# Performance work log

Hardware: AMD Instinct MI355X
Metric: run time of the kernel (lower is better)

The kernel has to match this reference:

```python
import jax, jax.numpy as jnp
import numpy as np
import math

EMBED_DIM = 512
NUM_CLASSES = 100000
BATCH = 1024
MARGIN = 0.5
SCALE = 64.0


def setup_inputs() -> dict:
    key = jax.random.key(0)
    k1, k2, k3 = jax.random.split(key, 3)
    embeddings = jax.random.normal(k1, (BATCH, EMBED_DIM), dtype=jnp.float32)
    labels = jax.random.randint(k2, (BATCH,), 0, NUM_CLASSES, dtype=jnp.int64)
    # xavier_uniform for weight [num_classes, embedding_dim]
    limit = math.sqrt(6.0 / (NUM_CLASSES + EMBED_DIM))
    weight = jax.random.uniform(k3, (NUM_CLASSES, EMBED_DIM), dtype=jnp.float32,
                                minval=-limit, maxval=limit)
    return {"embeddings": embeddings, "weight": weight, "labels": labels}


def _l2norm(x, axis=-1, eps=1e-12):
    # matches torch F.normalize (p=2, eps=1e-12)
    n = jnp.linalg.norm(x, axis=axis, keepdims=True)
    return x / jnp.maximum(n, eps)


def reference(embeddings, weight, labels):
    cos_m = math.cos(MARGIN)
    sin_m = math.sin(MARGIN)
    th = math.cos(math.pi - MARGIN)
    mm = math.sin(math.pi - MARGIN) * MARGIN

    # cosine similarity: [B, C]
    cosine = _l2norm(embeddings) @ _l2norm(weight).T
    sine = jnp.sqrt(jnp.clip(1.0 - cosine * cosine, 0.0, 1.0))
    phi = cosine * cos_m - sine * sin_m
    phi = jnp.where(cosine > th, phi, cosine - mm)

    # apply margin only at the label position
    one_hot = jax.nn.one_hot(labels, NUM_CLASSES, dtype=cosine.dtype)
    logits = SCALE * (one_hot * phi + (1.0 - one_hot) * cosine)

    # cross entropy, mean reduction
    logp = jax.nn.log_softmax(logits, axis=-1)
    nll = -jnp.take_along_axis(logp, labels[:, None], axis=1)[:, 0]
    return jnp.mean(nll)
```

## Files before the change

### kernel.cpp

```cpp
#include <hip/hip_runtime.h>
#include <hip/hip_bf16.h>
#include <math.h>

#define B_ROWS 1024
#define EMB    512
#define NCLS   100000
#define SCALE_ 64.0f
#define COS_M 0.8775825618903728f
#define SIN_M 0.479425538604203f
#define TH_C  (-0.8775825618903728f)
#define MM_C  0.2397127693021015f

#define BM 128
#define BN 128
#define BK 32
#define NTILES 782
#define KCHUNKS 16

#define NT2   391
#define GRID2 1564

typedef __attribute__((ext_vector_type(8))) short bf16x8;
typedef __attribute__((ext_vector_type(4))) short s16x4;
typedef __attribute__((ext_vector_type(4))) float f32x4;

typedef __attribute__((address_space(1))) const unsigned int GLP;
typedef __attribute__((address_space(3))) unsigned int LDP;

__device__ __forceinline__ float bf2f(short u) {
  unsigned int x = ((unsigned int)(unsigned short)u) << 16;
  return __builtin_bit_cast(float, x);
}
__device__ __forceinline__ short f2bf(float f) {
  unsigned int u = __builtin_bit_cast(unsigned int, f);
  u += 0x7FFF + ((u >> 16) & 1);
  return (short)(u >> 16);
}

__device__ __forceinline__ void load16(const void* g, void* l) {
  __builtin_amdgcn_global_load_lds((GLP*)g, (LDP*)l, 16, 0, 0);
}

__global__ void setup_kernel(const void* __restrict__ emb, const int* __restrict__ labels,
                             float* __restrict__ row_sum, float* __restrict__ accum,
                             int* __restrict__ flag, int* __restrict__ dflag) {
  const int t = threadIdx.x;
  row_sum[t] = 0.f;
  row_sum[t + 512] = 0.f;
  if (t == 0) *accum = 0.f;

  if (t < 64) {
    bf16x8 v = *(const bf16x8*)((const short*)emb + t * 8);
    float s = 0.f;
    #pragma unroll
    for (int j = 0; j < 8; ++j) { float f = bf2f(v[j]); s += f * f; }
    #pragma unroll
    for (int off = 1; off < 64; off <<= 1) s += __shfl_xor(s, off);
    if (t == 0) *dflag = (s < 1e8f) ? 1 : 0;
  }

  int v = labels[2 * t + 1];
  #pragma unroll
  for (int off = 1; off < 64; off <<= 1) v |= __shfl_xor(v, off);
  __shared__ int red[8];
  if ((t & 63) == 0) red[t >> 6] = v;
  __syncthreads();
  if (t == 0) {
    int o = 0;
    #pragma unroll
    for (int i = 0; i < 8; ++i) o |= red[i];
    *flag = (o == 0) ? 1 : 0;
  }
}

__global__ __launch_bounds__(256) void normconv_kernel(
    const void* __restrict__ emb, const void* __restrict__ wgt,
    const int* __restrict__ dflag,
    float* __restrict__ inv_e, float* __restrict__ inv_w,
    short* __restrict__ An, short* __restrict__ Wn, const int do_conv) {
  const int sub  = threadIdx.x & 15;
  const int rloc = threadIdx.x >> 4;
  const int row  = blockIdx.x * 16 + rloc;
  int r;
  const void* base;
  float* dst;
  short* out;
  if (row < B_ROWS) { r = row; base = emb; dst = inv_e + row; out = An + (size_t)row * EMB; }
  else {
    r = row - B_ROWS;
    if (r >= NCLS) return;
    base = wgt; dst = inv_w + r; out = Wn + (size_t)r * EMB;
  }
  const int isbf16 = *dflag;
  float f[32];
  if (isbf16) {
    const short* p = (const short*)base + (size_t)r * EMB;
    #pragma unroll
    for (int j = 0; j < 4; ++j) {
      bf16x8 v = *(const bf16x8*)(p + j * 128 + sub * 8);
      #pragma unroll
      for (int t = 0; t < 8; ++t) f[j * 8 + t] = bf2f(v[t]);
    }
  } else {
    const float* p = (const float*)base + (size_t)r * EMB;
    #pragma unroll
    for (int j = 0; j < 8; ++j) {
      f32x4 v = *(const f32x4*)(p + j * 64 + sub * 4);
      #pragma unroll
      for (int t = 0; t < 4; ++t) f[j * 4 + t] = v[t];
    }
  }
  float s = 0.f;
  #pragma unroll
  for (int j = 0; j < 32; ++j) s += f[j] * f[j];
  #pragma unroll
  for (int off = 1; off < 16; off <<= 1) s += __shfl_xor(s, off);
  const float inv = 1.f / fmaxf(sqrtf(s), 1e-12f);
  if (sub == 0) *dst = inv;
  if (do_conv) {
    if (isbf16) {
      #pragma unroll
      for (int j = 0; j < 4; ++j) {
        bf16x8 o;
        #pragma unroll
        for (int t = 0; t < 8; ++t) o[t] = f2bf(f[j * 8 + t] * inv);
        *(bf16x8*)(out + j * 128 + sub * 8) = o;
      }
    } else {
      #pragma unroll
      for (int j = 0; j < 8; ++j) {
        s16x4 o;
        #pragma unroll
        for (int t = 0; t < 4; ++t) o[t] = f2bf(f[j * 4 + t] * inv);
        *(s16x4*)(out + j * 64 + sub * 4) = o;
      }
    }
  }
}

__global__ __launch_bounds__(512, 2) void arc_gemm_fast(
    const short* __restrict__ A, const short* __restrict__ W,
    const int* __restrict__ labels, const int* __restrict__ flag,
    float* __restrict__ row_sum, float* __restrict__ lablogit) {
  const int bid = blockIdx.x;
  const int k   = bid & 7;
  const int jj  = bid >> 3;
  const int wgid = (k < 4 ? k * 196 : 4 * 196 + (k - 4) * 195) + jj;
  const int ytile = wgid >> 2;
  const int xtile = wgid & 3;
  if (ytile >= NT2) return;

  __shared__ __align__(16) char Lraw[131072 + 1024 + 4096];
  char* L = Lraw;
  int*   shl = (int*)(L + 131072);
  float* shs = (float*)(L + 131072 + 1024);

  const int tid  = threadIdx.x;
  const int wave = tid >> 6;
  const int lane = tid & 63;
  const int wm   = wave >> 2;
  const int wn   = wave & 3;
  const int lr16 = lane & 15;
  const int lkg  = lane >> 4;
  const int mBase = xtile * 256;
  const int nBase = ytile * 256;

  const char* Ab = (const char*)A;
  const char* Wb = (const char*)W;

  f32x4 zero = {0.f, 0.f, 0.f, 0.f};
  f32x4 acc[8][4];
  #pragma unroll
  for (int i = 0; i < 8; ++i)
    #pragma unroll
    for (int j2 = 0; j2 < 4; ++j2) acc[i][j2] = zero;

  auto stage = [&](int kt, int p) {
    #pragma unroll
    for (int j = 0; j < 4; ++j) {
      const int row = j * 64 + (tid >> 3);
      const int sl  = (tid & 7) ^ (row & 7);
      load16(Ab + (size_t)(mBase + row) * 1024 + kt * 128 + sl * 16,
             L + p * 65536 + j * 8192 + wave * 1024);
      int br = nBase + row;
      if (br >= NCLS) br = NCLS - 1;
      load16(Wb + (size_t)br * 1024 + kt * 128 + sl * 16,
             L + p * 65536 + 32768 + j * 8192 + wave * 1024);
    }
  };

  stage(0, 0);
  stage(1, 1);
  asm volatile("s_waitcnt vmcnt(8)" ::: "memory");
  __builtin_amdgcn_s_barrier();

  for (int t = 0; t < 8; ++t) {
    const int p = t & 1;
    const short* Abuf = (const short*)(L + p * 65536);
    const short* Bbuf = (const short*)(L + p * 65536 + 32768);
    bf16x8 af[2][8], bb[2][4];
    #pragma unroll
    for (int ks = 0; ks < 2; ++ks) {
      #pragma unroll
      for (int mi = 0; mi < 8; ++mi) {
        const int ra = wm * 128 + mi * 16 + lr16;
        const int sa = (ks * 4 + lkg) ^ (ra & 7);
        af[ks][mi] = *(const bf16x8*)(Abuf + ra * 64 + sa * 8);
      }
      #pragma unroll
      for (int ni = 0; ni < 4; ++ni) {
        const int rb = wn * 64 + ni * 16 + lr16;
        const int sb = (ks * 4 + lkg) ^ (rb & 7);
        bb[ks][ni] = *(const bf16x8*)(Bbuf + rb * 64 + sb * 8);
      }
    }
    asm volatile("s_waitcnt lgkmcnt(0)" ::: "memory");
    __builtin_amdgcn_s_barrier();
    stage((t + 2) & 7, p);
    __builtin_amdgcn_s_setprio(1);
    #pragma unroll
    for (int mi = 0; mi < 8; ++mi)
      #pragma unroll
      for (int ni = 0; ni < 4; ++ni) {
        acc[mi][ni] = __builtin_amdgcn_mfma_f32_16x16x32_bf16(af[0][mi], bb[0][ni], acc[mi][ni], 0, 0, 0);
        acc[mi][ni] = __builtin_amdgcn_mfma_f32_16x16x32_bf16(af[1][mi], bb[1][ni], acc[mi][ni], 0, 0, 0);
      }
    __builtin_amdgcn_s_setprio(0);
    asm volatile("s_waitcnt vmcnt(8)" ::: "memory");
    __builtin_amdgcn_s_barrier();
  }

  asm volatile("s_waitcnt vmcnt(0)" ::: "memory");
  __syncthreads();
  if (tid < 256) {
    const int r = mBase + tid;
    const int f = *flag;
    shl[tid] = labels[f ? (size_t)(2 * r) : (size_t)r];
  }
  __syncthreads();

  #pragma unroll
  for (int mi = 0; mi < 8; ++mi) {
    #pragma unroll
    for (int reg = 0; reg < 4; ++reg) {
      const int lrow = wm * 128 + mi * 16 + lkg * 4 + reg;
      const int grow = mBase + lrow;
      const int lab = shl[lrow];
      float s = 0.f;
      #pragma unroll
      for (int ni = 0; ni < 4; ++ni) {
        const int gcol = nBase + wn * 64 + ni * 16 + lr16;
        if (gcol < NCLS) {
          const float cosv = acc[mi][ni][reg];
          float logit;
          if (gcol == lab) {
            const float sine = sqrtf(fmaxf(1.f - cosv * cosv, 0.f));
            float phi = cosv * COS_M - sine * SIN_M;
            phi = (cosv > TH_C) ? phi : (cosv - MM_C);
            logit = SCALE_ * phi;
            lablogit[grow] = logit;
          } else {
            logit = SCALE_ * cosv;
          }
          s += __expf(logit - SCALE_);
        }
      }
      #pragma unroll
      for (int off = 1; off < 16; off <<= 1) s += __shfl_xor(s, off);
      if (lr16 == 0) shs[lrow * 4 + wn] = s;
    }
  }
  __syncthreads();
  if (tid < 256)
    atomicAdd(&row_sum[mBase + tid],
              shs[tid * 4] + shs[tid * 4 + 1] + shs[tid * 4 + 2] + shs[tid * 4 + 3]);
}

__global__ __launch_bounds__(256, 3) void arc_gemm(
    const void* __restrict__ A, const void* __restrict__ W,
    const float* __restrict__ inv_e, const float* __restrict__ inv_w,
    const int* __restrict__ labels, const int* __restrict__ flag,
    const int* __restrict__ dflag,
    float* __restrict__ row_sum, float* __restrict__ lablogit) {
  __shared__ short As[BM * BK];
  __shared__ short Bs[BN * BK];
  __shared__ int   sh_lab[BM];
  __shared__ float sh_sum[BM][2];

  const int tid  = threadIdx.x;
  const int wave = tid >> 6;
  const int lane = tid & 63;
  const int wy = wave >> 1;
  const int wx = wave & 1;
  const int lr = lane & 15;
  const int lk = lane >> 4;
  const int mBase = blockIdx.x * BM;
  const int nBase = blockIdx.y * BN;
  const int isbf16 = *dflag;

  const int srow  = lane >> 2;
  const int sbyte = (lane & 3) * 16;

  f32x4 zero = {0.f, 0.f, 0.f, 0.f};
  f32x4 acc[4][4];
  #pragma unroll
  for (int i = 0; i < 4; ++i)
    #pragma unroll
    for (int j = 0; j < 4; ++j) acc[i][j] = zero;

  const char*  Ab = (const char*)A;
  const char*  Wb = (const char*)W;
  const float* Af = (const float*)A;
  const float* Wf = (const float*)W;

  for (int kc = 0; kc < KCHUNKS; ++kc) {
    __syncthreads();
    if (isbf16) {
      const size_t koff = (size_t)kc * 64 + sbyte;
      #pragma unroll
      for (int it = 0; it < 2; ++it) {
        const int c = wave + it * 4;
        const int ar = mBase + c * 16 + srow;
        load16(Ab + (size_t)ar * 1024 + koff, (char*)As + (size_t)c * 1024);
        int br = nBase + c * 16 + srow;
        if (br >= NCLS) br = NCLS - 1;
        load16(Wb + (size_t)br * 1024 + koff, (char*)Bs + (size_t)c * 1024);
      }
    } else {
      #pragma unroll
      for (int p = 0; p < 2; ++p) {
        const int u   = p * 256 + tid;
        const int row = u >> 2;
        const int seg = u & 3;
        const float* ga = Af + ((size_t)(mBase + row) * EMB + kc * 32 + seg * 8);
        f32x4 x = *(const f32x4*)ga;
        f32x4 y = *(const f32x4*)(ga + 4);
        bf16x8 tpack;
        #pragma unroll
        for (int j = 0; j < 4; ++j) { tpack[j] = f2bf(x[j]); tpack[j + 4] = f2bf(y[j]); }
        *(bf16x8*)(As + row * BK + seg * 8) = tpack;
        int br = nBase + row;
        if (br >= NCLS) br = NCLS - 1;
        const float* gb = Wf + ((size_t)br * EMB + kc * 32 + seg * 8);
        x = *(const f32x4*)gb;
        y = *(const f32x4*)(gb + 4);
        #pragma unroll
        for (int j = 0; j < 4; ++j) { tpack[j] = f2bf(x[j]); tpack[j + 4] = f2bf(y[j]); }
        *(bf16x8*)(Bs + row * BK + seg * 8) = tpack;
      }
    }
    __syncthreads();
    bf16x8 af[4], bfr[4];
    #pragma unroll
    for (int mi = 0; mi < 4; ++mi)
      af[mi] = *(const bf16x8*)(As + ((wy * 64 + mi * 16 + lr) * BK + lk * 8));
    #pragma unroll
    for (int ni = 0; ni < 4; ++ni)
      bfr[ni] = *(const bf16x8*)(Bs + ((wx * 64 + ni * 16 + lr) * BK + lk * 8));
    #pragma unroll
    for (int mi = 0; mi < 4; ++mi)
      #pragma unroll
      for (int ni = 0; ni < 4; ++ni)
        acc[mi][ni] = __builtin_amdgcn_mfma_f32_16x16x32_bf16(af[mi], bfr[ni], acc[mi][ni], 0, 0, 0);
  }

  __syncthreads();
  if (tid < BM) {
    const int r = mBase + tid;
    const int f = *flag;
    sh_lab[tid] = labels[f ? (size_t)(2 * r) : (size_t)r];
  }
  __syncthreads();

  #pragma unroll
  for (int mi = 0; mi < 4; ++mi) {
    #pragma unroll
    for (int reg = 0; reg < 4; ++reg) {
      const int lrow = wy * 64 + mi * 16 + lk * 4 + reg;
      const int grow = mBase + lrow;
      const float ie = inv_e[grow];
      const int lab = sh_lab[lrow];
      float s = 0.f;
      #pragma unroll
      for (int ni = 0; ni < 4; ++ni) {
        const int gcol = nBase + wx * 64 + ni * 16 + lr;
        if (gcol < NCLS) {
          const float cosv = acc[mi][ni][reg] * ie * inv_w[gcol];
          float logit;
          if (gcol == lab) {
            const float sine = sqrtf(fmaxf(1.f - cosv * cosv, 0.f));
            float phi = cosv * COS_M - sine * SIN_M;
            phi = (cosv > TH_C) ? phi : (cosv - MM_C);
            logit = SCALE_ * phi;
            lablogit[grow] = logit;
          } else {
            logit = SCALE_ * cosv;
          }
          s += __expf(logit - SCALE_);
        }
      }
      #pragma unroll
      for (int off = 1; off < 16; off <<= 1) s += __shfl_xor(s, off);
      if (lr == 0) sh_sum[lrow][wx] = s;
    }
  }
  __syncthreads();
  if (tid < BM)
    atomicAdd(&row_sum[mBase + tid], sh_sum[tid][0] + sh_sum[tid][1]);
}

__global__ void loss_kernel(const float* __restrict__ row_sum,
                            const float* __restrict__ lablogit,
                            float* __restrict__ accum) {
  const int r = blockIdx.x * 128 + threadIdx.x;
  float loss = SCALE_ + logf(row_sum[r]) - lablogit[r];
  #pragma unroll
  for (int off = 1; off < 64; off <<= 1) loss += __shfl_xor(loss, off);
  __shared__ float rs[2];
  if ((threadIdx.x & 63) == 0) rs[threadIdx.x >> 6] = loss;
  __syncthreads();
  if (threadIdx.x == 0) atomicAdd(accum, rs[0] + rs[1]);
}

__global__ void finalize_kernel(const float* __restrict__ accum, float* __restrict__ out) {
  out[0] = accum[0] * (1.0f / 1024.0f);
}

extern "C" void kernel_launch(void* const* d_in, const int* in_sizes, int n_in,
                              void* d_out, int out_size, void* d_ws, size_t ws_size,
                              hipStream_t stream) {
  const void* emb   = d_in[0];
  const void* wgt   = d_in[1];
  const int* labels = (const int*)d_in[2];
  float* out = (float*)d_out;

  const int NORM_BLOCKS = (B_ROWS + NCLS + 15) / 16;

  const size_t WN_SHORTS = (size_t)NCLS * EMB;
  const size_t AN_SHORTS = (size_t)B_ROWS * EMB;
  const size_t FAST_NEED = (WN_SHORTS + AN_SHORTS) * 2 + 103075u * 4;

  if (ws_size >= FAST_NEED) {
    short* Wn = (short*)d_ws;
    short* An = Wn + WN_SHORTS;
    float* tail     = (float*)(An + AN_SHORTS);
    float* inv_e    = tail;
    float* inv_w    = tail + 1024;
    float* lablogit = tail + 101024;
    float* row_sum  = tail + 102048;
    float* accum    = tail + 103072;
    int*   flag     = (int*)(tail + 103073);
    int*   dflag    = (int*)(tail + 103074);

    setup_kernel<<<1, 512, 0, stream>>>(emb, labels, row_sum, accum, flag, dflag);
    normconv_kernel<<<NORM_BLOCKS, 256, 0, stream>>>(
        emb, wgt, dflag, inv_e, inv_w, An, Wn, 1);
    arc_gemm_fast<<<GRID2, 512, 0, stream>>>(An, Wn, labels, flag, row_sum, lablogit);
    loss_kernel<<<8, 128, 0, stream>>>(row_sum, lablogit, accum);
    finalize_kernel<<<1, 1, 0, stream>>>(accum, out);
  } else {
    float* ws       = (float*)d_ws;
    float* inv_e    = ws;
    float* inv_w    = ws + 1024;
    float* lablogit = ws + 101024;
    float* row_sum  = ws + 102048;
    float* accum    = ws + 103072;
    int*   flag     = (int*)(ws + 103073);
    int*   dflag    = (int*)(ws + 103074);

    setup_kernel<<<1, 512, 0, stream>>>(emb, labels, row_sum, accum, flag, dflag);
    normconv_kernel<<<NORM_BLOCKS, 256, 0, stream>>>(
        emb, wgt, dflag, inv_e, inv_w, (short*)inv_e, (short*)inv_e, 0);
    dim3 grid(8, NTILES);
    arc_gemm<<<grid, 256, 0, stream>>>(emb, wgt, inv_e, inv_w, labels, flag, dflag, row_sum, lablogit);
    loss_kernel<<<8, 128, 0, stream>>>(row_sum, lablogit, accum);
    finalize_kernel<<<1, 1, 0, stream>>>(accum, out);
  }
}
```

Baseline: 495.3 us.

## Split GEMM k-step into four quadrant phases interleaving LDS reads, prefetch, MFMA

Restructures the main k-loop of the fast GEMM so that each k-tile runs as four sub-phases. Each phase loads half of the A or B fragments from LDS, issues a quarter of the next tile's global-to-LDS copies, then runs its MFMA block. This lowers register pressure from fragments and spreads memory traffic across the compute instead of bursting it. It also merges the loss and finalize kernels into one single-block kernel, removing a launch and an atomic. The cost is more barriers per k-step and trickier vmcnt accounting.

```diff
diff --git a/kernel.cpp b/kernel.cpp
--- a/kernel.cpp
+++ b/kernel.cpp
@@ -40,6 +40,10 @@
 __device__ __forceinline__ void load16(const void* g, void* l) {
   __builtin_amdgcn_global_load_lds((GLP*)g, (LDP*)l, 16, 0, 0);
 }
+
+#define MFMA16 __builtin_amdgcn_mfma_f32_16x16x32_bf16
+#define WAITLG do { asm volatile("s_waitcnt lgkmcnt(0)" ::: "memory"); \
+                    __builtin_amdgcn_sched_barrier(0); } while (0)
 
 __global__ void setup_kernel(const void* __restrict__ emb, const int* __restrict__ labels,
                              float* __restrict__ row_sum, float* __restrict__ accum,
@@ -150,8 +154,7 @@
   const int xtile = wgid & 3;
   if (ytile >= NT2) return;
 
-  __shared__ __align__(16) char Lraw[131072 + 1024 + 4096];
-  char* L = Lraw;
+  __shared__ __align__(16) char L[131072 + 1024 + 4096];
   int*   shl = (int*)(L + 131072);
   float* shs = (float*)(L + 131072 + 1024);
 
@@ -168,6 +171,27 @@
   const char* Ab = (const char*)A;
   const char* Wb = (const char*)W;
 
+  const int sslot = (tid & 7) ^ ((tid >> 3) & 7);
+
+  auto stage_one = [&](int s, int ii) {
+    const int pp = s & 1;
+    const int rloc = (ii & 3) * 64 + (tid >> 3);
+    const char* src;
+    if (ii < 4) {
+      src = Ab + (size_t)(mBase + rloc) * 1024 + (size_t)s * 128 + sslot * 16;
+    } else {
+      int br = nBase + rloc;
+      if (br >= NCLS) br = NCLS - 1;
+      src = Wb + (size_t)br * 1024 + (size_t)s * 128 + sslot * 16;
+    }
+    load16(src, L + pp * 65536 + ii * 8192 + wave * 1024);
+  };
+  auto stage_pair = [&](int s, int l) {
+    if ((unsigned)(s - 2) > 5u) return;
+    stage_one(s, 2 * l);
+    stage_one(s, 2 * l + 1);
+  };
+
   f32x4 zero = {0.f, 0.f, 0.f, 0.f};
   f32x4 acc[8][4];
   #pragma unroll
@@ -175,62 +199,107 @@
     #pragma unroll
     for (int j2 = 0; j2 < 4; ++j2) acc[i][j2] = zero;
 
-  auto stage = [&](int kt, int p) {
-    #pragma unroll
-    for (int j = 0; j < 4; ++j) {
-      const int row = j * 64 + (tid >> 3);
-      const int sl  = (tid & 7) ^ (row & 7);
-      load16(Ab + (size_t)(mBase + row) * 1024 + kt * 128 + sl * 16,
-             L + p * 65536 + j * 8192 + wave * 1024);
-      int br = nBase + row;
-      if (br >= NCLS) br = NCLS - 1;
-      load16(Wb + (size_t)br * 1024 + kt * 128 + sl * 16,
-             L + p * 65536 + 32768 + j * 8192 + wave * 1024);
-    }
-  };
-
-  stage(0, 0);
-  stage(1, 1);
+  const int slA  = lkg ^ (lr16 & 7);
+  const int slB  = slA ^ 4;
+
+  #pragma unroll
+  for (int ii = 0; ii < 8; ++ii) stage_one(0, ii);
+  #pragma unroll
+  for (int ii = 0; ii < 8; ++ii) stage_one(1, ii);
   asm volatile("s_waitcnt vmcnt(8)" ::: "memory");
   __builtin_amdgcn_s_barrier();
 
+  bf16x8 af0[4], af1[4];
+  bf16x8 b01[2][2], b23[2][2];
+
   for (int t = 0; t < 8; ++t) {
     const int p = t & 1;
-    const short* Abuf = (const short*)(L + p * 65536);
-    const short* Bbuf = (const short*)(L + p * 65536 + 32768);
-    bf16x8 af[2][8], bb[2][4];
-    #pragma unroll
-    for (int ks = 0; ks < 2; ++ks) {
-      #pragma unroll
-      for (int mi = 0; mi < 8; ++mi) {
-        const int ra = wm * 128 + mi * 16 + lr16;
-        const int sa = (ks * 4 + lkg) ^ (ra & 7);
-        af[ks][mi] = *(const bf16x8*)(Abuf + ra * 64 + sa * 8);
-      }
-      #pragma unroll
-      for (int ni = 0; ni < 4; ++ni) {
-        const int rb = wn * 64 + ni * 16 + lr16;
-        const int sb = (ks * 4 + lkg) ^ (rb & 7);
-        bb[ks][ni] = *(const bf16x8*)(Bbuf + rb * 64 + sb * 8);
-      }
-    }
-    asm volatile("s_waitcnt lgkmcnt(0)" ::: "memory");
-    __builtin_amdgcn_s_barrier();
-    stage((t + 2) & 7, p);
+    const short* AL = (const short*)(L + p * 65536);
+    const short* BL = (const short*)(L + p * 65536 + 32768);
+
+    #pragma unroll
+    for (int mi = 0; mi < 4; ++mi) {
+      const int row = wm * 128 + mi * 16 + lr16;
+      af0[mi] = *(const bf16x8*)(AL + row * 64 + slA * 8);
+      af1[mi] = *(const bf16x8*)(AL + row * 64 + slB * 8);
+    }
+    #pragma unroll
+    for (int ni = 0; ni < 2; ++ni) {
+      const int row = wn * 64 + ni * 16 + lr16;
+      b01[0][ni] = *(const bf16x8*)(BL + row * 64 + slA * 8);
+      b01[1][ni] = *(const bf16x8*)(BL + row * 64 + slB * 8);
+    }
+    stage_pair(t + 1, 1);
+    __builtin_amdgcn_s_barrier();
     __builtin_amdgcn_s_setprio(1);
     #pragma unroll
-    for (int mi = 0; mi < 8; ++mi)
-      #pragma unroll
-      for (int ni = 0; ni < 4; ++ni) {
-        acc[mi][ni] = __builtin_amdgcn_mfma_f32_16x16x32_bf16(af[0][mi], bb[0][ni], acc[mi][ni], 0, 0, 0);
-        acc[mi][ni] = __builtin_amdgcn_mfma_f32_16x16x32_bf16(af[1][mi], bb[1][ni], acc[mi][ni], 0, 0, 0);
+    for (int mi = 0; mi < 4; ++mi)
+      #pragma unroll
+      for (int ni = 0; ni < 2; ++ni) {
+        acc[mi][ni] = MFMA16(af0[mi], b01[0][ni], acc[mi][ni], 0, 0, 0);
+        acc[mi][ni] = MFMA16(af1[mi], b01[1][ni], acc[mi][ni], 0, 0, 0);
       }
     __builtin_amdgcn_s_setprio(0);
-    asm volatile("s_waitcnt vmcnt(8)" ::: "memory");
-    __builtin_amdgcn_s_barrier();
-  }
-
-  asm volatile("s_waitcnt vmcnt(0)" ::: "memory");
+    WAITLG;
+    __builtin_amdgcn_s_barrier();
+
+    #pragma unroll
+    for (int ni = 0; ni < 2; ++ni) {
+      const int row = wn * 64 + (ni + 2) * 16 + lr16;
+      b23[0][ni] = *(const bf16x8*)(BL + row * 64 + slA * 8);
+      b23[1][ni] = *(const bf16x8*)(BL + row * 64 + slB * 8);
+    }
+    stage_pair(t + 1, 2);
+    __builtin_amdgcn_s_barrier();
+    __builtin_amdgcn_s_setprio(1);
+    #pragma unroll
+    for (int mi = 0; mi < 4; ++mi)
+      #pragma unroll
+      for (int ni = 0; ni < 2; ++ni) {
+        acc[mi][ni + 2] = MFMA16(af0[mi], b23[0][ni], acc[mi][ni + 2], 0, 0, 0);
+        acc[mi][ni + 2] = MFMA16(af1[mi], b23[1][ni], acc[mi][ni + 2], 0, 0, 0);
+      }
+    __builtin_amdgcn_s_setprio(0);
+    WAITLG;
+    __builtin_amdgcn_s_barrier();
+
+    #pragma unroll
+    for (int mi = 0; mi < 4; ++mi) {
+      const int row = wm * 128 + (mi + 4) * 16 + lr16;
+      af0[mi] = *(const bf16x8*)(AL + row * 64 + slA * 8);
+      af1[mi] = *(const bf16x8*)(AL + row * 64 + slB * 8);
+    }
+    stage_pair(t + 1, 3);
+    __builtin_amdgcn_s_barrier();
+    __builtin_amdgcn_s_setprio(1);
+    #pragma unroll
+    for (int mi = 0; mi < 4; ++mi)
+      #pragma unroll
+      for (int ni = 0; ni < 2; ++ni) {
+        acc[mi + 4][ni + 2] = MFMA16(af0[mi], b23[0][ni], acc[mi + 4][ni + 2], 0, 0, 0);
+        acc[mi + 4][ni + 2] = MFMA16(af1[mi], b23[1][ni], acc[mi + 4][ni + 2], 0, 0, 0);
+      }
+    __builtin_amdgcn_s_setprio(0);
+    WAITLG;
+    __builtin_amdgcn_s_barrier();
+
+    stage_pair(t + 2, 0);
+    __builtin_amdgcn_s_barrier();
+    __builtin_amdgcn_s_setprio(1);
+    #pragma unroll
+    for (int mi = 0; mi < 4; ++mi)
+      #pragma unroll
+      for (int ni = 0; ni < 2; ++ni) {
+        acc[mi + 4][ni] = MFMA16(af0[mi], b01[0][ni], acc[mi + 4][ni], 0, 0, 0);
+        acc[mi + 4][ni] = MFMA16(af1[mi], b01[1][ni], acc[mi + 4][ni], 0, 0, 0);
+      }
+    __builtin_amdgcn_s_setprio(0);
+    WAITLG;
+    if (t < 6)      asm volatile("s_waitcnt vmcnt(2)" ::: "memory");
+    else if (t == 6) asm volatile("s_waitcnt vmcnt(0)" ::: "memory");
+    __builtin_amdgcn_s_barrier();
+  }
+
   __syncthreads();
   if (tid < 256) {
     const int r = mBase + tid;
@@ -361,7 +430,7 @@
     for (int mi = 0; mi < 4; ++mi)
       #pragma unroll
       for (int ni = 0; ni < 4; ++ni)
-        acc[mi][ni] = __builtin_amdgcn_mfma_f32_16x16x32_bf16(af[mi], bfr[ni], acc[mi][ni], 0, 0, 0);
+        acc[mi][ni] = MFMA16(af[mi], bfr[ni], acc[mi][ni], 0, 0, 0);
   }
 
   __syncthreads();
@@ -409,21 +478,27 @@
     atomicAdd(&row_sum[mBase + tid], sh_sum[tid][0] + sh_sum[tid][1]);
 }
 
-__global__ void loss_kernel(const float* __restrict__ row_sum,
-                            const float* __restrict__ lablogit,
-                            float* __restrict__ accum) {
-  const int r = blockIdx.x * 128 + threadIdx.x;
-  float loss = SCALE_ + logf(row_sum[r]) - lablogit[r];
+__global__ __launch_bounds__(512) void loss_kernel(const float* __restrict__ row_sum,
+                                                   const float* __restrict__ lablogit,
+                                                   float* __restrict__ out) {
+  const int t = threadIdx.x;
+  float loss = 0.f;
+  #pragma unroll
+  for (int i = 0; i < 2; ++i) {
+    const int r = t + i * 512;
+    loss += SCALE_ + logf(row_sum[r]) - lablogit[r];
+  }
   #pragma unroll
   for (int off = 1; off < 64; off <<= 1) loss += __shfl_xor(loss, off);
-  __shared__ float rs[2];
-  if ((threadIdx.x & 63) == 0) rs[threadIdx.x >> 6] = loss;
-  __syncthreads();
-  if (threadIdx.x == 0) atomicAdd(accum, rs[0] + rs[1]);
-}
-
-__global__ void finalize_kernel(const float* __restrict__ accum, float* __restrict__ out) {
-  out[0] = accum[0] * (1.0f / 1024.0f);
+  __shared__ float rs[8];
+  if ((t & 63) == 0) rs[t >> 6] = loss;
+  __syncthreads();
+  if (t == 0) {
+    float s = 0.f;
+    #pragma unroll
+    for (int i = 0; i < 8; ++i) s += rs[i];
+    out[0] = s * (1.0f / 1024.0f);
+  }
 }
 
 extern "C" void kernel_launch(void* const* d_in, const int* in_sizes, int n_in,
@@ -456,8 +531,7 @@
     normconv_kernel<<<NORM_BLOCKS, 256, 0, stream>>>(
         emb, wgt, dflag, inv_e, inv_w, An, Wn, 1);
     arc_gemm_fast<<<GRID2, 512, 0, stream>>>(An, Wn, labels, flag, row_sum, lablogit);
-    loss_kernel<<<8, 128, 0, stream>>>(row_sum, lablogit, accum);
-    finalize_kernel<<<1, 1, 0, stream>>>(accum, out);
+    loss_kernel<<<1, 512, 0, stream>>>(row_sum, lablogit, out);
   } else {
     float* ws       = (float*)d_ws;
     float* inv_e    = ws;
@@ -473,7 +547,6 @@
         emb, wgt, dflag, inv_e, inv_w, (short*)inv_e, (short*)inv_e, 0);
     dim3 grid(8, NTILES);
     arc_gemm<<<grid, 256, 0, stream>>>(emb, wgt, inv_e, inv_w, labels, flag, dflag, row_sum, lablogit);
-    loss_kernel<<<8, 128, 0, stream>>>(row_sum, lablogit, accum);
-    finalize_kernel<<<1, 1, 0, stream>>>(accum, out);
-  }
-}
+    loss_kernel<<<1, 512, 0, stream>>>(row_sum, lablogit, out);
+  }
+}
```

After: 482.0 us. 1.03x faster.
